# Kernel tuning notes

Measured on AMD Instinct MI355X. Metric: run time of the kernel, lower is better.

## Reference

```python
import jax, jax.numpy as jnp
import numpy as np

EPS = 1e-08
NUM_EMBEDDINGS = 8192
EMBEDDING_DIM = 256
N_TOKENS = 32768


def setup_inputs() -> dict:
    key = jax.random.key(0)
    k1, k2, k3 = jax.random.split(key, 3)
    input_data = jax.random.normal(k1, (N_TOKENS, EMBEDDING_DIM), dtype=jnp.float32)
    rand = jax.random.normal(k2, (N_TOKENS, EMBEDDING_DIM), dtype=jnp.float32)
    codebooks = jax.random.normal(k3, (NUM_EMBEDDINGS, EMBEDDING_DIM), dtype=jnp.float32)
    return {"input_data": input_data, "rand": rand, "codebooks": codebooks}


def reference(input_data, rand, codebooks):
    # d2: (N, K) -- this full matrix is what a fused kernel would avoid.
    d2 = (jnp.sum(input_data * input_data, axis=1, keepdims=True)
          - 2.0 * input_data @ codebooks.T
          + jnp.sum(codebooks * codebooks, axis=1)[None, :])
    min_idx = jnp.argmin(d2, axis=1)                      # (N,)
    hard_q = codebooks[min_idx]                           # (N, D)

    # Noise substitution: scale unit-ish gaussian noise to the residual norm.
    r_norm = jnp.linalg.norm(input_data - hard_q, axis=1, keepdims=True)
    n_norm = jnp.linalg.norm(rand, axis=1, keepdims=True)
    quantized_input = input_data + (r_norm / (n_norm + EPS)) * rand

    # Perplexity from codebook usage counts (no grad path in original).
    counts = jnp.zeros((NUM_EMBEDDINGS,), dtype=jnp.float32).at[min_idx].add(1.0)
    total = jnp.maximum(counts.sum(), 1.0)
    avg_probs = counts / total
    perplexity = jnp.exp(-jnp.sum(avg_probs * jnp.log(avg_probs + EPS)))
    num_unique_indices = jnp.sum(counts > 0).astype(jnp.int32)
    return quantized_input, perplexity, num_unique_indices
```

## Files before the change

kernel.cpp:

```cpp
#include <hip/hip_runtime.h>
#include <stdint.h>

#define N_TOKENS 32768
#define N_CODES  8192
#define DIM      256
#define EPSF     1e-8f

typedef __bf16 bf16x8 __attribute__((ext_vector_type(8)));
typedef float  f32x4  __attribute__((ext_vector_type(4)));

#define WS_CNORM_OFF  (4u*1024u*1024u)
#define WS_HIST_OFF   (WS_CNORM_OFF + N_CODES*4u)

__global__ __launch_bounds__(256) void k_prep(const float* __restrict__ cbf,
                                              unsigned short* __restrict__ cbh,
                                              float* __restrict__ cnorm,
                                              int* __restrict__ hist) {
    const int tid = blockIdx.x * 256 + threadIdx.x;
    if (tid < N_CODES) hist[tid] = 0;

    const int w = threadIdx.x >> 6;
    const int lane = threadIdx.x & 63;
    const int row = blockIdx.x * 4 + w;

    const float4 v = ((const float4*)(cbf + (size_t)row * DIM))[lane];
    float sq = v.x * v.x + v.y * v.y + v.z * v.z + v.w * v.w;

    ushort4 u;
    u.x = __builtin_bit_cast(unsigned short, (__bf16)v.x);
    u.y = __builtin_bit_cast(unsigned short, (__bf16)v.y);
    u.z = __builtin_bit_cast(unsigned short, (__bf16)v.z);
    u.w = __builtin_bit_cast(unsigned short, (__bf16)v.w);
    ((ushort4*)(cbh + (size_t)row * DIM))[lane] = u;

    #pragma unroll
    for (int d = 1; d < 64; d <<= 1) sq += __shfl_xor(sq, d);
    if (lane == 0) cnorm[row] = sq;
}

__global__ __launch_bounds__(512, 2) void k_argmin(const float* __restrict__ X,
                                                   const float* __restrict__ R,
                                                   const unsigned short* __restrict__ cbh,
                                                   const float* __restrict__ cnorm,
                                                   float* __restrict__ out,
                                                   int* __restrict__ hist) {
    __shared__ __attribute__((aligned(16))) char smem[87040];
    float* cnS   = (float*)(smem + 65536);
    float* redv  = (float*)(smem + 66048);
    int*   redi  = (int*)(smem + 68096);
    float* maxvS = (float*)(smem + 70144);

    const int tid  = threadIdx.x;
    const int w    = tid >> 6;
    const int lane = tid & 63;
    const int lr   = lane & 15;
    const int lq   = lane >> 4;
    const int th   = w >> 2;
    const int wc   = w & 3;
    const int r0   = blockIdx.x * 128;
    const int mycol = wc * 16 + lr;

    {
        const float4* Xf4 = (const float4*)(X + (size_t)(r0 + 16 * w) * DIM);
        #pragma unroll
        for (int i = 0; i < 16; ++i) {
            const float4 v = Xf4[i * 64 + lane];
            ushort4 u;
            u.x = __builtin_bit_cast(unsigned short, (__bf16)v.x);
            u.y = __builtin_bit_cast(unsigned short, (__bf16)v.y);
            u.z = __builtin_bit_cast(unsigned short, (__bf16)v.z);
            u.w = __builtin_bit_cast(unsigned short, (__bf16)v.w);
            *(ushort4*)(smem + (16 * w + i) * 544 + lane * 8) = u;
        }
    }
    __syncthreads();

    bf16x8 A[4][8];
    #pragma unroll
    for (int mf = 0; mf < 4; ++mf)
        #pragma unroll
        for (int kc = 0; kc < 8; ++kc)
            A[mf][kc] = *(const bf16x8*)(smem + (64 * th + mf * 16 + lr) * 544 + kc * 64 + lq * 16);
    __syncthreads();

    const int half = lane >> 5, l5 = lane & 31;
    int srcoff[4];
    #pragma unroll
    for (int s = 0; s < 4; ++s) {
        const int c = 8 * w + 2 * s + half;
        const int j = (l5 - c) & 31;
        srcoff[s] = c * 512 + j * 16;
    }
    const char* cbb = (const char*)cbh;

    #pragma unroll
    for (int s = 0; s < 4; ++s)
        __builtin_amdgcn_global_load_lds(
            (const __attribute__((address_space(1))) unsigned int*)(cbb + srcoff[s]),
            (__attribute__((address_space(3))) unsigned int*)(smem + w * 4096 + s * 1024),
            16, 0, 0);
    if (w == 0)
        __builtin_amdgcn_global_load_lds(
            (const __attribute__((address_space(1))) unsigned int*)(cnorm + lane),
            (__attribute__((address_space(3))) unsigned int*)(cnS),
            4, 0, 0);
    __syncthreads();

    float maxv[16];
    int   maxi[16];
    #pragma unroll
    for (int i = 0; i < 16; ++i) { maxv[i] = -3.4e38f; maxi[i] = 0; }

    for (int cc = 0; cc < 128; ++cc) {
        const int cur = (cc & 1) * 32768;
        if (cc + 1 < 128) {
            const int nxt = ((cc + 1) & 1) * 32768;
            const char* src = cbb + (size_t)(cc + 1) * 32768;
            #pragma unroll
            for (int s = 0; s < 4; ++s)
                __builtin_amdgcn_global_load_lds(
                    (const __attribute__((address_space(1))) unsigned int*)(src + srcoff[s]),
                    (__attribute__((address_space(3))) unsigned int*)(smem + nxt + w * 4096 + s * 1024),
                    16, 0, 0);
            if (w == 0)
                __builtin_amdgcn_global_load_lds(
                    (const __attribute__((address_space(1))) unsigned int*)(cnorm + (cc + 1) * 64 + lane),
                    (__attribute__((address_space(3))) unsigned int*)(cnS + ((cc + 1) & 1) * 64),
                    4, 0, 0);
        }

        const float cinit = -0.5f * cnS[(cc & 1) * 64 + mycol];
        f32x4 acc[4];
        #pragma unroll
        for (int mf = 0; mf < 4; ++mf) {
            acc[mf][0] = cinit; acc[mf][1] = cinit; acc[mf][2] = cinit; acc[mf][3] = cinit;
        }

        #pragma unroll
        for (int kc = 0; kc < 8; ++kc) {
            const bf16x8 b = *(const bf16x8*)(smem + cur + mycol * 512 +
                                              (((kc * 4 + lq + mycol) & 31) << 4));
            #pragma unroll
            for (int mf = 0; mf < 4; ++mf)
                acc[mf] = __builtin_amdgcn_mfma_f32_16x16x32_bf16(A[mf][kc], b, acc[mf], 0, 0, 0);
        }

        const int col = cc * 64 + mycol;
        #pragma unroll
        for (int mf = 0; mf < 4; ++mf)
            #pragma unroll
            for (int r = 0; r < 4; ++r) {
                const float v = acc[mf][r];
                const int j = mf * 4 + r;
                if (v > maxv[j]) { maxv[j] = v; maxi[j] = col; }
            }

        __syncthreads();
    }

    #pragma unroll
    for (int mf = 0; mf < 4; ++mf)
        #pragma unroll
        for (int r = 0; r < 4; ++r) {
            float v = maxv[mf * 4 + r]; int ix = maxi[mf * 4 + r];
            #pragma unroll
            for (int d = 1; d <= 8; d <<= 1) {
                const float ov = __shfl_xor(v, d);
                const int   oi = __shfl_xor(ix, d);
                if (ov > v || (ov == v && oi < ix)) { v = ov; ix = oi; }
            }
            if (lr == 0) {
                const int row = mf * 16 + lq * 4 + r;
                redv[w * 64 + row] = v; redi[w * 64 + row] = ix;
            }
        }
    __syncthreads();

    if (tid < 128) {
        const int t = tid, tth = t >> 6, tl = t & 63;
        float v = redv[(4 * tth) * 64 + tl]; int ix = redi[(4 * tth) * 64 + tl];
        #pragma unroll
        for (int ww = 1; ww < 4; ++ww) {
            const float ov = redv[(4 * tth + ww) * 64 + tl];
            const int   oi = redi[(4 * tth + ww) * 64 + tl];
            if (ov > v || (ov == v && oi < ix)) { v = ov; ix = oi; }
        }
        maxvS[t] = v;
        atomicAdd(&hist[ix], 1);
    }
    __syncthreads();

    for (int i = 0; i < 16; ++i) {
        const int tl = 16 * w + i;
        const int tok = r0 + tl;
        const float4 x = ((const float4*)(X + (size_t)tok * DIM))[lane];
        const float4 r = ((const float4*)(R + (size_t)tok * DIM))[lane];

        float x2 = x.x * x.x + x.y * x.y + x.z * x.z + x.w * x.w;
        float n2 = r.x * r.x + r.y * r.y + r.z * r.z + r.w * r.w;
        #pragma unroll
        for (int d = 1; d < 64; d <<= 1) {
            x2 += __shfl_xor(x2, d);
            n2 += __shfl_xor(n2, d);
        }
        const float mv = maxvS[tl];
        const float d2 = fmaxf(fmaf(-2.f, mv, x2), 0.f);
        const float s = sqrtf(d2) / (sqrtf(n2) + EPSF);

        float4 o;
        o.x = fmaf(s, r.x, x.x);
        o.y = fmaf(s, r.y, x.y);
        o.z = fmaf(s, r.z, x.z);
        o.w = fmaf(s, r.w, x.w);
        ((float4*)(out + (size_t)tok * DIM))[lane] = o;
    }
}

__global__ __launch_bounds__(1024) void k_stats(const int* __restrict__ hist,
                                                float* __restrict__ outs) {
    float s = 0.f; int u = 0;
    for (int b = threadIdx.x; b < N_CODES; b += 1024) {
        const float c = (float)hist[b];
        if (c > 0.f) ++u;
        const float p = c * (1.f / (float)N_TOKENS);
        s += p * logf(p + EPSF);
    }
    #pragma unroll
    for (int d = 1; d < 64; d <<= 1) {
        s += __shfl_xor(s, d);
        u += __shfl_xor(u, d);
    }
    __shared__ float ss[16];
    __shared__ int   su[16];
    const int w = threadIdx.x >> 6, lane = threadIdx.x & 63;
    if (lane == 0) { ss[w] = s; su[w] = u; }
    __syncthreads();
    if (threadIdx.x == 0) {
        float st = 0.f; int ut = 0;
        #pragma unroll
        for (int i = 0; i < 16; ++i) { st += ss[i]; ut += su[i]; }
        outs[0] = expf(-st);
        outs[1] = (float)ut;
    }
}

extern "C" void kernel_launch(void* const* d_in, const int* in_sizes, int n_in,
                              void* d_out, int out_size, void* d_ws, size_t ws_size,
                              hipStream_t stream) {
    const float* X = (const float*)d_in[0];
    const float* R = (const float*)d_in[1];
    const float* C = (const float*)d_in[2];
    float* out = (float*)d_out;

    char* ws = (char*)d_ws;
    unsigned short* cbh = (unsigned short*)ws;
    float* cnorm = (float*)(ws + WS_CNORM_OFF);
    int*   hist  = (int*)(ws + WS_HIST_OFF);

    k_prep  <<<N_CODES / 4,    256, 0, stream>>>(C, cbh, cnorm, hist);
    k_argmin<<<N_TOKENS / 128, 512, 0, stream>>>(X, R, cbh, cnorm, out, hist);
    k_stats <<<1, 1024, 0, stream>>>(hist, out + (size_t)N_TOKENS * DIM);
}
```

Before: 246.4 us.

## Triple-buffer codebook tiles in LDS with vmcnt-based partial waits

New measurement: 258.6 us. 1.05x slower.

```diff
diff --git a/kernel.cpp b/kernel.cpp
--- a/kernel.cpp
+++ b/kernel.cpp
@@ -44,11 +44,11 @@
                                                    const float* __restrict__ cnorm,
                                                    float* __restrict__ out,
                                                    int* __restrict__ hist) {
-    __shared__ __attribute__((aligned(16))) char smem[87040];
-    float* cnS   = (float*)(smem + 65536);
-    float* redv  = (float*)(smem + 66048);
-    int*   redi  = (int*)(smem + 68096);
-    float* maxvS = (float*)(smem + 70144);
+    __shared__ __attribute__((aligned(16))) char smem[103680];
+    float* cnS   = (float*)(smem + 98304);
+    float* redv  = (float*)(smem + 99072);
+    int*   redi  = (int*)(smem + 101120);
+    float* maxvS = (float*)(smem + 103168);
 
     const int tid  = threadIdx.x;
     const int w    = tid >> 6;
@@ -94,48 +94,60 @@
     const char* cbb = (const char*)cbh;
 
     #pragma unroll
-    for (int s = 0; s < 4; ++s)
-        __builtin_amdgcn_global_load_lds(
-            (const __attribute__((address_space(1))) unsigned int*)(cbb + srcoff[s]),
-            (__attribute__((address_space(3))) unsigned int*)(smem + w * 4096 + s * 1024),
-            16, 0, 0);
-    if (w == 0)
-        __builtin_amdgcn_global_load_lds(
-            (const __attribute__((address_space(1))) unsigned int*)(cnorm + lane),
-            (__attribute__((address_space(3))) unsigned int*)(cnS),
-            4, 0, 0);
-    __syncthreads();
+    for (int p = 0; p < 2; ++p) {
+        const char* src = cbb + (size_t)p * 32768;
+        #pragma unroll
+        for (int s = 0; s < 4; ++s)
+            __builtin_amdgcn_global_load_lds(
+                (const __attribute__((address_space(1))) unsigned int*)(src + srcoff[s]),
+                (__attribute__((address_space(3))) unsigned int*)(smem + p * 32768 + w * 4096 + s * 1024),
+                16, 0, 0);
+        if (w == 0)
+            __builtin_amdgcn_global_load_lds(
+                (const __attribute__((address_space(1))) unsigned int*)(cnorm + p * 64 + lane),
+                (__attribute__((address_space(3))) unsigned int*)(cnS + p * 64),
+                4, 0, 0);
+    }
 
     float maxv[16];
     int   maxi[16];
     #pragma unroll
     for (int i = 0; i < 16; ++i) { maxv[i] = -3.4e38f; maxi[i] = 0; }
 
+    int cur = 0;
     for (int cc = 0; cc < 128; ++cc) {
-        const int cur = (cc & 1) * 32768;
-        if (cc + 1 < 128) {
-            const int nxt = ((cc + 1) & 1) * 32768;
-            const char* src = cbb + (size_t)(cc + 1) * 32768;
+        if (cc == 127) {
+            asm volatile("s_waitcnt vmcnt(0)\n\ts_barrier" ::: "memory");
+        } else if (w == 0) {
+            asm volatile("s_waitcnt vmcnt(5)\n\ts_barrier" ::: "memory");
+        } else {
+            asm volatile("s_waitcnt vmcnt(4)\n\ts_barrier" ::: "memory");
+        }
+
+        if (cc + 2 < 128) {
+            int stg = cur + 65536; if (stg >= 98304) stg -= 98304;
+            const char* src = cbb + (size_t)(cc + 2) * 32768;
             #pragma unroll
             for (int s = 0; s < 4; ++s)
                 __builtin_amdgcn_global_load_lds(
                     (const __attribute__((address_space(1))) unsigned int*)(src + srcoff[s]),
-                    (__attribute__((address_space(3))) unsigned int*)(smem + nxt + w * 4096 + s * 1024),
+                    (__attribute__((address_space(3))) unsigned int*)(smem + stg + w * 4096 + s * 1024),
                     16, 0, 0);
             if (w == 0)
                 __builtin_amdgcn_global_load_lds(
-                    (const __attribute__((address_space(1))) unsigned int*)(cnorm + (cc + 1) * 64 + lane),
-                    (__attribute__((address_space(3))) unsigned int*)(cnS + ((cc + 1) & 1) * 64),
+                    (const __attribute__((address_space(1))) unsigned int*)(cnorm + (cc + 2) * 64 + lane),
+                    (__attribute__((address_space(3))) unsigned int*)(cnS + (stg >> 9)),
                     4, 0, 0);
         }
 
-        const float cinit = -0.5f * cnS[(cc & 1) * 64 + mycol];
+        const float cinit = -0.5f * cnS[(cur >> 9) + mycol];
         f32x4 acc[4];
         #pragma unroll
         for (int mf = 0; mf < 4; ++mf) {
             acc[mf][0] = cinit; acc[mf][1] = cinit; acc[mf][2] = cinit; acc[mf][3] = cinit;
         }
 
+        __builtin_amdgcn_s_setprio(1);
         #pragma unroll
         for (int kc = 0; kc < 8; ++kc) {
             const bf16x8 b = *(const bf16x8*)(smem + cur + mycol * 512 +
@@ -144,6 +156,7 @@
             for (int mf = 0; mf < 4; ++mf)
                 acc[mf] = __builtin_amdgcn_mfma_f32_16x16x32_bf16(A[mf][kc], b, acc[mf], 0, 0, 0);
         }
+        __builtin_amdgcn_s_setprio(0);
 
         const int col = cc * 64 + mycol;
         #pragma unroll
@@ -155,7 +168,7 @@
                 if (v > maxv[j]) { maxv[j] = v; maxi[j] = col; }
             }
 
-        __syncthreads();
+        cur += 32768; if (cur >= 98304) cur -= 98304;
     }
 
     #pragma unroll
```

## Load codebook tiles directly from global into registers, drop LDS double-buffer

Applied to the files above, without the earlier changes.

Measured after the change: 360.5 us. 1.46x slower.

```diff
diff --git a/kernel.cpp b/kernel.cpp
--- a/kernel.cpp
+++ b/kernel.cpp
@@ -44,11 +44,10 @@
                                                    const float* __restrict__ cnorm,
                                                    float* __restrict__ out,
                                                    int* __restrict__ hist) {
-    __shared__ __attribute__((aligned(16))) char smem[87040];
-    float* cnS   = (float*)(smem + 65536);
-    float* redv  = (float*)(smem + 66048);
-    int*   redi  = (int*)(smem + 68096);
-    float* maxvS = (float*)(smem + 70144);
+    __shared__ __attribute__((aligned(16))) char smem[74240];
+    float* redv  = (float*)(smem + 69632);
+    int*   redi  = (int*)(smem + 71680);
+    float* maxvS = (float*)(smem + 73728);
 
     const int tid  = threadIdx.x;
     const int w    = tid >> 6;
@@ -81,55 +80,22 @@
         #pragma unroll
         for (int kc = 0; kc < 8; ++kc)
             A[mf][kc] = *(const bf16x8*)(smem + (64 * th + mf * 16 + lr) * 544 + kc * 64 + lq * 16);
-    __syncthreads();
-
-    const int half = lane >> 5, l5 = lane & 31;
-    int srcoff[4];
-    #pragma unroll
-    for (int s = 0; s < 4; ++s) {
-        const int c = 8 * w + 2 * s + half;
-        const int j = (l5 - c) & 31;
-        srcoff[s] = c * 512 + j * 16;
-    }
-    const char* cbb = (const char*)cbh;
-
-    #pragma unroll
-    for (int s = 0; s < 4; ++s)
-        __builtin_amdgcn_global_load_lds(
-            (const __attribute__((address_space(1))) unsigned int*)(cbb + srcoff[s]),
-            (__attribute__((address_space(3))) unsigned int*)(smem + w * 4096 + s * 1024),
-            16, 0, 0);
-    if (w == 0)
-        __builtin_amdgcn_global_load_lds(
-            (const __attribute__((address_space(1))) unsigned int*)(cnorm + lane),
-            (__attribute__((address_space(3))) unsigned int*)(cnS),
-            4, 0, 0);
-    __syncthreads();
 
     float maxv[16];
     int   maxi[16];
     #pragma unroll
     for (int i = 0; i < 16; ++i) { maxv[i] = -3.4e38f; maxi[i] = 0; }
 
+    const char* bsrc = (const char*)cbh + (size_t)mycol * 512 + (size_t)lq * 16;
+    const float* cnp = cnorm + mycol;
+
     for (int cc = 0; cc < 128; ++cc) {
-        const int cur = (cc & 1) * 32768;
-        if (cc + 1 < 128) {
-            const int nxt = ((cc + 1) & 1) * 32768;
-            const char* src = cbb + (size_t)(cc + 1) * 32768;
-            #pragma unroll
-            for (int s = 0; s < 4; ++s)
-                __builtin_amdgcn_global_load_lds(
-                    (const __attribute__((address_space(1))) unsigned int*)(src + srcoff[s]),
-                    (__attribute__((address_space(3))) unsigned int*)(smem + nxt + w * 4096 + s * 1024),
-                    16, 0, 0);
-            if (w == 0)
-                __builtin_amdgcn_global_load_lds(
-                    (const __attribute__((address_space(1))) unsigned int*)(cnorm + (cc + 1) * 64 + lane),
-                    (__attribute__((address_space(3))) unsigned int*)(cnS + ((cc + 1) & 1) * 64),
-                    4, 0, 0);
-        }
-
-        const float cinit = -0.5f * cnS[(cc & 1) * 64 + mycol];
+        bf16x8 b[8];
+        #pragma unroll
+        for (int kc = 0; kc < 8; ++kc)
+            b[kc] = *(const bf16x8*)(bsrc + (size_t)cc * 32768 + kc * 64);
+
+        const float cinit = -0.5f * cnp[(size_t)cc * 64];
         f32x4 acc[4];
         #pragma unroll
         for (int mf = 0; mf < 4; ++mf) {
@@ -137,13 +103,10 @@
         }
 
         #pragma unroll
-        for (int kc = 0; kc < 8; ++kc) {
-            const bf16x8 b = *(const bf16x8*)(smem + cur + mycol * 512 +
-                                              (((kc * 4 + lq + mycol) & 31) << 4));
+        for (int kc = 0; kc < 8; ++kc)
             #pragma unroll
             for (int mf = 0; mf < 4; ++mf)
-                acc[mf] = __builtin_amdgcn_mfma_f32_16x16x32_bf16(A[mf][kc], b, acc[mf], 0, 0, 0);
-        }
+                acc[mf] = __builtin_amdgcn_mfma_f32_16x16x32_bf16(A[mf][kc], b[kc], acc[mf], 0, 0, 0);
 
         const int col = cc * 64 + mycol;
         #pragma unroll
@@ -154,8 +117,6 @@
                 const int j = mf * 4 + r;
                 if (v > maxv[j]) { maxv[j] = v; maxi[j] = col; }
             }
-
-        __syncthreads();
     }
 
     #pragma unroll
```

## Split codebook chunk into two phases with barriers, setprio, and deferred argmin

Applied to the files above, without the earlier changes.

Result: slower. 264.0 us (+7.2%).

```diff
diff --git a/kernel.cpp b/kernel.cpp
--- a/kernel.cpp
+++ b/kernel.cpp
@@ -44,11 +44,11 @@
                                                    const float* __restrict__ cnorm,
                                                    float* __restrict__ out,
                                                    int* __restrict__ hist) {
-    __shared__ __attribute__((aligned(16))) char smem[87040];
+    __shared__ __attribute__((aligned(16))) char smem[102912];
     float* cnS   = (float*)(smem + 65536);
-    float* redv  = (float*)(smem + 66048);
-    int*   redi  = (int*)(smem + 68096);
-    float* maxvS = (float*)(smem + 70144);
+    float* redv  = (float*)(smem + 98304);
+    int*   redi  = (int*)(smem + 100352);
+    float* maxvS = (float*)(smem + 102400);
 
     const int tid  = threadIdx.x;
     const int w    = tid >> 6;
@@ -93,69 +93,126 @@
     }
     const char* cbb = (const char*)cbh;
 
-    #pragma unroll
-    for (int s = 0; s < 4; ++s)
-        __builtin_amdgcn_global_load_lds(
-            (const __attribute__((address_space(1))) unsigned int*)(cbb + srcoff[s]),
-            (__attribute__((address_space(3))) unsigned int*)(smem + w * 4096 + s * 1024),
-            16, 0, 0);
-    if (w == 0)
-        __builtin_amdgcn_global_load_lds(
-            (const __attribute__((address_space(1))) unsigned int*)(cnorm + lane),
-            (__attribute__((address_space(3))) unsigned int*)(cnS),
-            4, 0, 0);
-    __syncthreads();
+    {
+        const char* cnb = (const char*)cnorm;
+        #pragma unroll
+        for (int i = 0; i < 4; ++i)
+            __builtin_amdgcn_global_load_lds(
+                (const __attribute__((address_space(1))) unsigned int*)(cnb + i * 8192 + tid * 16),
+                (__attribute__((address_space(3))) unsigned int*)(smem + 65536 + i * 8192 + tid * 16),
+                16, 0, 0);
+        #pragma unroll
+        for (int s = 0; s < 4; ++s)
+            __builtin_amdgcn_global_load_lds(
+                (const __attribute__((address_space(1))) unsigned int*)(cbb + srcoff[s]),
+                (__attribute__((address_space(3))) unsigned int*)(smem + w * 4096 + s * 1024),
+                16, 0, 0);
+    }
 
     float maxv[16];
     int   maxi[16];
+    f32x4 acc[4];
     #pragma unroll
     for (int i = 0; i < 16; ++i) { maxv[i] = -3.4e38f; maxi[i] = 0; }
+    #pragma unroll
+    for (int mf = 0; mf < 4; ++mf) {
+        acc[mf][0] = -3.4e38f; acc[mf][1] = -3.4e38f;
+        acc[mf][2] = -3.4e38f; acc[mf][3] = -3.4e38f;
+    }
 
     for (int cc = 0; cc < 128; ++cc) {
-        const int cur = (cc & 1) * 32768;
+        const int cur = (cc & 1) << 15;
+        const int nxt = ((cc + 1) & 1) << 15;
+        const char* nsrc = cbb + (size_t)(cc + 1) * 32768;
+
+        asm volatile("s_waitcnt vmcnt(0)\n\ts_barrier" ::: "memory");
+
         if (cc + 1 < 128) {
-            const int nxt = ((cc + 1) & 1) * 32768;
-            const char* src = cbb + (size_t)(cc + 1) * 32768;
-            #pragma unroll
-            for (int s = 0; s < 4; ++s)
+            #pragma unroll
+            for (int s = 0; s < 2; ++s)
                 __builtin_amdgcn_global_load_lds(
-                    (const __attribute__((address_space(1))) unsigned int*)(src + srcoff[s]),
+                    (const __attribute__((address_space(1))) unsigned int*)(nsrc + srcoff[s]),
                     (__attribute__((address_space(3))) unsigned int*)(smem + nxt + w * 4096 + s * 1024),
                     16, 0, 0);
-            if (w == 0)
+        }
+        bf16x8 b0[4];
+        #pragma unroll
+        for (int kc = 0; kc < 4; ++kc)
+            b0[kc] = *(const bf16x8*)(smem + cur + mycol * 512 +
+                                      (((kc * 4 + lq + mycol) & 31) << 4));
+        const float cinit = -0.5f * cnS[cc * 64 + mycol];
+
+        {
+            const int pcol = (cc - 1) * 64 + mycol;
+            #pragma unroll
+            for (int mf = 0; mf < 4; ++mf)
+                #pragma unroll
+                for (int r = 0; r < 4; ++r) {
+                    const float v = acc[mf][r];
+                    const int j = mf * 4 + r;
+                    if (v > maxv[j]) { maxv[j] = v; maxi[j] = pcol; }
+                }
+        }
+        #pragma unroll
+        for (int mf = 0; mf < 4; ++mf) {
+            acc[mf][0] = cinit; acc[mf][1] = cinit;
+            acc[mf][2] = cinit; acc[mf][3] = cinit;
+        }
+
+        __builtin_amdgcn_sched_barrier(0);
+        __builtin_amdgcn_s_barrier();
+        __builtin_amdgcn_sched_barrier(0);
+
+        __builtin_amdgcn_s_setprio(1);
+        #pragma unroll
+        for (int kc = 0; kc < 4; ++kc)
+            #pragma unroll
+            for (int mf = 0; mf < 4; ++mf)
+                acc[mf] = __builtin_amdgcn_mfma_f32_16x16x32_bf16(A[mf][kc], b0[kc], acc[mf], 0, 0, 0);
+        __builtin_amdgcn_s_setprio(0);
+
+        __builtin_amdgcn_sched_barrier(0);
+        __builtin_amdgcn_s_barrier();
+        __builtin_amdgcn_sched_barrier(0);
+
+        if (cc + 1 < 128) {
+            #pragma unroll
+            for (int s = 2; s < 4; ++s)
                 __builtin_amdgcn_global_load_lds(
-                    (const __attribute__((address_space(1))) unsigned int*)(cnorm + (cc + 1) * 64 + lane),
-                    (__attribute__((address_space(3))) unsigned int*)(cnS + ((cc + 1) & 1) * 64),
-                    4, 0, 0);
-        }
-
-        const float cinit = -0.5f * cnS[(cc & 1) * 64 + mycol];
-        f32x4 acc[4];
-        #pragma unroll
-        for (int mf = 0; mf < 4; ++mf) {
-            acc[mf][0] = cinit; acc[mf][1] = cinit; acc[mf][2] = cinit; acc[mf][3] = cinit;
-        }
-
-        #pragma unroll
-        for (int kc = 0; kc < 8; ++kc) {
-            const bf16x8 b = *(const bf16x8*)(smem + cur + mycol * 512 +
-                                              (((kc * 4 + lq + mycol) & 31) << 4));
+                    (const __attribute__((address_space(1))) unsigned int*)(nsrc + srcoff[s]),
+                    (__attribute__((address_space(3))) unsigned int*)(smem + nxt + w * 4096 + s * 1024),
+                    16, 0, 0);
+        }
+        bf16x8 b1[4];
+        #pragma unroll
+        for (int kc = 4; kc < 8; ++kc)
+            b1[kc - 4] = *(const bf16x8*)(smem + cur + mycol * 512 +
+                                          (((kc * 4 + lq + mycol) & 31) << 4));
+
+        __builtin_amdgcn_sched_barrier(0);
+        __builtin_amdgcn_s_barrier();
+        __builtin_amdgcn_sched_barrier(0);
+
+        __builtin_amdgcn_s_setprio(1);
+        #pragma unroll
+        for (int kc = 0; kc < 4; ++kc)
             #pragma unroll
             for (int mf = 0; mf < 4; ++mf)
-                acc[mf] = __builtin_amdgcn_mfma_f32_16x16x32_bf16(A[mf][kc], b, acc[mf], 0, 0, 0);
-        }
-
-        const int col = cc * 64 + mycol;
+                acc[mf] = __builtin_amdgcn_mfma_f32_16x16x32_bf16(A[mf][kc + 4], b1[kc], acc[mf], 0, 0, 0);
+        __builtin_amdgcn_s_setprio(0);
+        __builtin_amdgcn_sched_barrier(0);
+    }
+
+    {
+        const int pcol = 127 * 64 + mycol;
         #pragma unroll
         for (int mf = 0; mf < 4; ++mf)
             #pragma unroll
             for (int r = 0; r < 4; ++r) {
                 const float v = acc[mf][r];
                 const int j = mf * 4 + r;
-                if (v > maxv[j]) { maxv[j] = v; maxi[j] = col; }
+                if (v > maxv[j]) { maxv[j] = v; maxi[j] = pcol; }
             }
-
-        __syncthreads();
     }
 
     #pragma unroll
```
